# Kernel optimization log

Measured on AMD Instinct MI355X. Metric: run time of the kernel, lower is better.

The kernel has to match this reference:

```python
import jax, jax.numpy as jnp
import numpy as np

N = 50000   # nodes
E = 800000  # edges (avg degree 16)
G = 32      # graphs in batch
IN = 128; HID = 64; H = 2; C = 16
NEG_SLOPE = 0.2
BN_EPS = 1e-5


def setup_inputs() -> dict:
    key = jax.random.key(0)
    ks = jax.random.split(key, 16)
    def rn(k, shape, scale=0.1):
        return jax.random.normal(k, shape, jnp.float32) * scale
    return {
        "feat": jax.random.normal(ks[0], (N, IN), jnp.float32),
        "W0": rn(ks[1], (IN, H * HID)),
        "attn0": rn(ks[2], (H, HID)),
        "W1": rn(ks[3], (H * HID, H * HID)),
        "attn1": rn(ks[4], (H, HID)),
        "W2": rn(ks[5], (H * HID, H * HID)),
        "attn2": rn(ks[6], (H, HID)),
        "Wf": rn(ks[7], (H * HID, H * C)),
        "attnf": rn(ks[8], (H, C)),
        "mlp_w1": rn(ks[9], (C, C)),
        "mlp_gamma": jnp.ones((C,), jnp.float32),
        "mlp_beta": jnp.zeros((C,), jnp.float32),
        "mlp_w2": rn(ks[10], (C, C)),
        "src": jax.random.randint(ks[11], (E,), 0, N, jnp.int32),
        "dst": jax.random.randint(ks[12], (E,), 0, N, jnp.int32),
        "node_graph": jnp.sort(jax.random.randint(ks[13], (N,), 0, G, jnp.int32)),
        "num_graphs": G,
    }


def gatv2_layer(h, src, dst, W, attn, act):
    """DGL GATv2Conv with share_weights=True, bias=False, residual=False."""
    n = h.shape[0]
    nh, d = attn.shape
    z = (h @ W).reshape(n, nh, d)                      # [N,H,D]
    zs = z[src]                                        # [E,H,D] gather (src)
    e = jax.nn.leaky_relu(zs + z[dst], NEG_SLOPE)      # [E,H,D]
    score = jnp.einsum('ehd,hd->eh', e, attn)          # [E,H]
    # edge softmax over incoming edges of dst (shift-invariant max trick)
    m = jax.lax.stop_gradient(jax.ops.segment_max(score, dst, num_segments=n))
    a = jnp.exp(score - m[dst])
    denom = jax.ops.segment_sum(a, dst, num_segments=n)[dst]
    alpha = a / jnp.where(denom == 0, 1.0, denom)      # [E,H]
    out = jax.ops.segment_sum(alpha[..., None] * zs, dst, num_segments=n)  # [N,H,D]
    return act(out) if act is not None else out


def reference(feat, W0, attn0, W1, attn1, W2, attn2, Wf, attnf,
              mlp_w1, mlp_gamma, mlp_beta, mlp_w2,
              src, dst, node_graph, num_graphs):
    relu = jax.nn.relu
    n = feat.shape[0]
    h = gatv2_layer(feat, src, dst, W0, attn0, relu).reshape(n, -1)
    h = gatv2_layer(h, src, dst, W1, attn1, relu).reshape(n, -1)
    h = gatv2_layer(h, src, dst, W2, attn2, relu).reshape(n, -1)
    logits = gatv2_layer(h, src, dst, Wf, attnf, None).mean(axis=1)  # [N,C]
    pooled = jax.ops.segment_sum(logits, node_graph, num_segments=num_graphs)  # [G,C]
    # MLP: relu(batchnorm(lin0(x))) -> lin1 (training-mode batch stats, biased var)
    h1 = pooled @ mlp_w1
    mu = h1.mean(axis=0)
    var = h1.var(axis=0)
    h1 = (h1 - mu) / jnp.sqrt(var + BN_EPS) * mlp_gamma + mlp_beta
    out = relu(h1) @ mlp_w2
    return jax.nn.log_softmax(out, axis=-1)
```

## Files before the change

### kernel.cpp

```cpp
#include <hip/hip_runtime.h>
#include <hip/hip_bf16.h>
#include <hip/hip_fp16.h>
#include <math.h>

#define NN 50000
#define EE 800000
#define GG 32
#define HD 64
#define NHEAD 2
#define CCLS 16
#define NEG_SLOPE 0.2f
#define BN_EPS 1e-5f
#define LOG2E 1.4426950408889634f
#define STRIDE 64

typedef unsigned int u32;
typedef unsigned short u16;
typedef _Float16 hv2 __attribute__((ext_vector_type(2)));
typedef __fp16   cv2 __attribute__((ext_vector_type(2)));

__device__ __forceinline__ hv2 bch2(u32 u) { union { u32 u; hv2 h; } c; c.u = u; return c.h; }
__device__ __forceinline__ u32 bcu32(hv2 h) { union { hv2 h; u32 u; } c; c.h = h; return c.u; }
__device__ __forceinline__ u32 pkrtz(float a, float b) {
    cv2 r = __builtin_amdgcn_cvt_pkrtz(a, b);
    union { cv2 h; u32 u; } c; c.h = r; return c.u;
}
__device__ __forceinline__ hv2 h2max(hv2 a, hv2 b) {
    return __builtin_elementwise_max(a, b);
}
__device__ __forceinline__ float fdot2(hv2 a, hv2 b, float c) {
#if __has_builtin(__builtin_amdgcn_fdot2)
    union { hv2 h; cv2 c2; } ua, ub;
    ua.h = a; ub.h = b;
    return __builtin_amdgcn_fdot2(ua.c2, ub.c2, c, false);
#else
    return fmaf((float)a[0], (float)b[0], fmaf((float)a[1], (float)b[1], c));
#endif
}


__global__ __launch_bounds__(256) void scatter_kernel(const int* __restrict__ src,
                                                      const int* __restrict__ dst,
                                                      int* __restrict__ cursor,
                                                      u16* __restrict__ csr_src) {
    int e = blockIdx.x * 256 + threadIdx.x;
    if (e < EE) {
        int d = dst[e];
        int s = src[e];
        int p = atomicAdd(&cursor[d], 1);
        csr_src[d * STRIDE + p] = (u16)s;
    }
}


template<int KOUT, int RPT, bool F16IN>
__device__ __forceinline__ void gemm_body(const void* __restrict__ hv,
                                          const float* __restrict__ W,
                                          u32* __restrict__ z, int n, int blk) {
    constexpr int CT = KOUT / 8;
    constexpr int RT = 256 / CT;
    constexpr int BR = RT * RPT;
    constexpr int WSTR = (KOUT == 128) ? 140 : (KOUT + 4);
    __shared__ __align__(16) u32 WpD[64 * WSTR];
    __shared__ __align__(16) uint4 hsU4[BR * 17];
    int t = threadIdx.x;
    int row0 = blk * BR;

    for (int i = t; i < 64 * (KOUT / 4); i += 256) {
        int k2 = i / (KOUT / 4), cq = i % (KOUT / 4);
        float4 wa = ((const float4*)W)[(2 * k2) * (KOUT / 4) + cq];
        float4 wb = ((const float4*)W)[(2 * k2 + 1) * (KOUT / 4) + cq];
        uint4 d;
        d.x = pkrtz(wa.x, wb.x); d.y = pkrtz(wa.y, wb.y);
        d.z = pkrtz(wa.z, wb.z); d.w = pkrtz(wa.w, wb.w);
        *(uint4*)&WpD[k2 * WSTR + 4 * cq + ((cq >> 3) << 2)] = d;
    }
    for (int i = t; i < BR * 16; i += 256) {
        int r = i >> 4, c16 = i & 15;
        int gr = row0 + r;
        uint4 u = {0, 0, 0, 0};
        if (gr < n) {
            if (F16IN) {
                u = ((const uint4*)hv)[(size_t)gr * 16 + c16];
            } else {
                float4 f0 = ((const float4*)hv)[(size_t)gr * 32 + 2 * c16];
                float4 f1 = ((const float4*)hv)[(size_t)gr * 32 + 2 * c16 + 1];
                u.x = pkrtz(f0.x, f0.y); u.y = pkrtz(f0.z, f0.w);
                u.z = pkrtz(f1.x, f1.y); u.w = pkrtz(f1.z, f1.w);
            }
        }
        hsU4[r * 17 + c16] = u;
    }
    __syncthreads();

    int tc = t % CT, tr = t / CT;
    float acc[RPT][8];
    #pragma unroll
    for (int i = 0; i < RPT; i++)
        #pragma unroll
        for (int c = 0; c < 8; c++) acc[i][c] = 0.f;

    for (int kq = 0; kq < 16; kq++) {
        uint4 a4[RPT];
        #pragma unroll
        for (int i = 0; i < RPT; i++) a4[i] = hsU4[(tr * RPT + i) * 17 + kq];
        #pragma unroll
        for (int j = 0; j < 4; j++) {
            const u32* wrow = &WpD[(4 * kq + j) * WSTR + tc * 8 + ((tc >> 2) << 2)];
            uint4 wa = *(const uint4*)wrow;
            uint4 wb = *(const uint4*)(wrow + 4);
            u32 wd[8] = {wa.x, wa.y, wa.z, wa.w, wb.x, wb.y, wb.z, wb.w};
            #pragma unroll
            for (int i = 0; i < RPT; i++) {
                u32 av[4] = {a4[i].x, a4[i].y, a4[i].z, a4[i].w};
                hv2 a2 = bch2(av[j]);
                #pragma unroll
                for (int c = 0; c < 8; c++)
                    acc[i][c] = fdot2(a2, bch2(wd[c]), acc[i][c]);
            }
        }
    }
    #pragma unroll
    for (int i = 0; i < RPT; i++) {
        int gr = row0 + tr * RPT + i;
        if (gr < n) {
            uint4 p;
            p.x = pkrtz(acc[i][0], acc[i][1]);
            p.y = pkrtz(acc[i][2], acc[i][3]);
            p.z = pkrtz(acc[i][4], acc[i][5]);
            p.w = pkrtz(acc[i][6], acc[i][7]);
            ((uint4*)z)[(size_t)gr * (KOUT / 8) + tc] = p;
        }
    }
}

template<int KOUT, int RPT, bool F16IN>
__global__ __launch_bounds__(256) void gemm_kernel(const void* __restrict__ hv,
                                                   const float* __restrict__ W,
                                                   u32* __restrict__ z, int n) {
    gemm_body<KOUT, RPT, F16IN>(hv, W, z, n, blockIdx.x);
}

__global__ __launch_bounds__(256) void gemm0_kernel(const void* __restrict__ hv,
                                                    const float* __restrict__ W,
                                                    u32* __restrict__ z,
                                                    int* __restrict__ cursor,
                                                    float* __restrict__ pooled) {
    int gid = blockIdx.x * 256 + threadIdx.x;
    if (gid < NN) cursor[gid] = 0;
    if (gid < GG * CCLS) pooled[gid] = 0.f;
    gemm_body<128, 4, false>(hv, W, z, NN, blockIdx.x);
}


__global__ __launch_bounds__(256) void edge_kernel(const u32* __restrict__ z,
                                                   const float* __restrict__ attn,
                                                   const int* __restrict__ cursor,
                                                   const u16* __restrict__ csr_src,
                                                   u32* __restrict__ out, int n) {
    int wave = blockIdx.x * 4 + (threadIdx.x >> 6);
    int lane = threadIdx.x & 63;
    if (wave >= n) return;
    int i = wave;
    int slot = lane >> 3;
    int q8 = lane & 7;
    const uint4* zr = (const uint4*)z;

    size_t rowi = (size_t)i * 16 + q8 * 2;
    uint4 zua = zr[rowi], zub = zr[rowi + 1];
    hv2 zd[8] = {bch2(zua.x), bch2(zua.y), bch2(zua.z), bch2(zua.w),
                 bch2(zub.x), bch2(zub.y), bch2(zub.z), bch2(zub.w)};
    const float4* af = (const float4*)attn;
    float4 a0 = af[q8 * 4 + 0], a1 = af[q8 * 4 + 1];
    float4 a2 = af[q8 * 4 + 2], a3 = af[q8 * 4 + 3];
    hv2 ah[8] = {bch2(pkrtz(a0.x * LOG2E, a0.y * LOG2E)),
                 bch2(pkrtz(a0.z * LOG2E, a0.w * LOG2E)),
                 bch2(pkrtz(a1.x * LOG2E, a1.y * LOG2E)),
                 bch2(pkrtz(a1.z * LOG2E, a1.w * LOG2E)),
                 bch2(pkrtz(a2.x * LOG2E, a2.y * LOG2E)),
                 bch2(pkrtz(a2.z * LOG2E, a2.w * LOG2E)),
                 bch2(pkrtz(a3.x * LOG2E, a3.y * LOG2E)),
                 bch2(pkrtz(a3.z * LOG2E, a3.w * LOG2E))};
    const hv2 slope2 = {(_Float16)NEG_SLOPE, (_Float16)NEG_SLOPE};

    int deg = cursor[i];
    const u16* ep = csr_src + i * STRIDE;

    float s = 0.f;
    float accf[16];
    #pragma unroll
    for (int j = 0; j < 16; j++) accf[j] = 0.f;

    bool valid = slot < deg;
    int sid = valid ? (int)ep[slot] : i;
    size_t rs = (size_t)sid * 16 + q8 * 2;
    uint4 sa = zr[rs], sb = zr[rs + 1];

    for (int k = 0; k < deg; k += 8) {
        bool more = (k + 8) < deg;
        bool v2 = (k + 8 + slot) < deg;
        uint4 na, nb;
        if (more) {
            int sid2 = v2 ? (int)ep[k + 8 + slot] : i;
            size_t rs2 = (size_t)sid2 * 16 + q8 * 2;
            na = zr[rs2]; nb = zr[rs2 + 1];
        }
        hv2 zs[8] = {bch2(sa.x), bch2(sa.y), bch2(sa.z), bch2(sa.w),
                     bch2(sb.x), bch2(sb.y), bch2(sb.z), bch2(sb.w)};
        float sc = 0.f;
        #pragma unroll
        for (int j = 0; j < 8; j++) {
            hv2 x = zs[j] + zd[j];
            x = h2max(x, x * slope2);
            sc = fdot2(x, ah[j], sc);
        }
        sc += __shfl_xor(sc, 2, 64);
        sc += __shfl_xor(sc, 1, 64);
        float p = valid ? exp2f(sc) : 0.f;
        s += p;
        #pragma unroll
        for (int j = 0; j < 8; j++) {
            accf[2 * j]     = fmaf(p, (float)zs[j][0], accf[2 * j]);
            accf[2 * j + 1] = fmaf(p, (float)zs[j][1], accf[2 * j + 1]);
        }
        sa = na; sb = nb; valid = v2;
    }

    u32 pk[8];
    #pragma unroll
    for (int j = 0; j < 8; j++) pk[j] = pkrtz(accf[2 * j], accf[2 * j + 1]);
    #pragma unroll
    for (int off = 8; off <= 32; off <<= 1) {
        s += __shfl_xor(s, off, 64);
        #pragma unroll
        for (int j = 0; j < 8; j++) {
            u32 o = (u32)__shfl_xor((int)pk[j], off, 64);
            pk[j] = bcu32(bch2(pk[j]) + bch2(o));
        }
    }

    if (slot == 0) {
        float inv = s > 0.f ? 1.f / s : 0.f;
        hv2 inv2 = bch2(pkrtz(inv, inv));
        const hv2 zero2 = {(_Float16)0.f, (_Float16)0.f};
        uint4 pa, pb;
        pa.x = bcu32(h2max(bch2(pk[0]) * inv2, zero2));
        pa.y = bcu32(h2max(bch2(pk[1]) * inv2, zero2));
        pa.z = bcu32(h2max(bch2(pk[2]) * inv2, zero2));
        pa.w = bcu32(h2max(bch2(pk[3]) * inv2, zero2));
        pb.x = bcu32(h2max(bch2(pk[4]) * inv2, zero2));
        pb.y = bcu32(h2max(bch2(pk[5]) * inv2, zero2));
        pb.z = bcu32(h2max(bch2(pk[6]) * inv2, zero2));
        pb.w = bcu32(h2max(bch2(pk[7]) * inv2, zero2));
        ((uint4*)out)[rowi] = pa;
        ((uint4*)out)[rowi + 1] = pb;
    }
}


__global__ __launch_bounds__(256) void edge_final_kernel(const u32* __restrict__ z,
                                                         const float* __restrict__ attn,
                                                         const int* __restrict__ cursor,
                                                         const u16* __restrict__ csr_src,
                                                         const int* __restrict__ node_graph,
                                                         float* __restrict__ pooled, int n) {
    __shared__ float pl[GG * CCLS];
    for (int t = threadIdx.x; t < GG * CCLS; t += 256) pl[t] = 0.f;
    __syncthreads();

    int wave = blockIdx.x * 4 + (threadIdx.x >> 6);
    int lane = threadIdx.x & 63;
    int iv = wave * 2 + (lane >> 5);
    bool mine = iv < n;
    int i = mine ? iv : (n - 1);
    int hl = lane & 31;
    int j = hl >> 3;
    int d8 = hl & 7;
    const uint2* zr = (const uint2*)z;
    uint2 zu = zr[(size_t)i * 8 + d8];
    hv2 zd0 = bch2(zu.x), zd1 = bch2(zu.y);
    float4 av = ((const float4*)attn)[d8];
    hv2 ah0 = bch2(pkrtz(av.x * LOG2E, av.y * LOG2E));
    hv2 ah1 = bch2(pkrtz(av.z * LOG2E, av.w * LOG2E));
    const hv2 slope2 = {(_Float16)NEG_SLOPE, (_Float16)NEG_SLOPE};
    int deg = cursor[i];
    const u16* ep = csr_src + i * STRIDE;

    float s = 0.f;
    float accf[4] = {0.f, 0.f, 0.f, 0.f};
    for (int k = 0; k < deg; k += 4) {
        int kk = k + j;
        bool valid = kk < deg;
        int sid = valid ? (int)ep[kk] : i;
        uint2 su = zr[(size_t)sid * 8 + d8];
        hv2 zs0 = bch2(su.x), zs1 = bch2(su.y);
        hv2 x;
        float sc = 0.f;
        x = zs0 + zd0; x = h2max(x, x * slope2); sc = fdot2(x, ah0, sc);
        x = zs1 + zd1; x = h2max(x, x * slope2); sc = fdot2(x, ah1, sc);
        sc += __shfl_xor(sc, 1, 64);
        sc += __shfl_xor(sc, 2, 64);
        float p = valid ? exp2f(sc) : 0.f;
        s += p;
        accf[0] = fmaf(p, (float)zs0[0], accf[0]);
        accf[1] = fmaf(p, (float)zs0[1], accf[1]);
        accf[2] = fmaf(p, (float)zs1[0], accf[2]);
        accf[3] = fmaf(p, (float)zs1[1], accf[3]);
    }
    #pragma unroll
    for (int off = 8; off <= 16; off <<= 1) {
        s += __shfl_xor(s, off, 64);
        #pragma unroll
        for (int jj = 0; jj < 4; jj++) accf[jj] += __shfl_xor(accf[jj], off, 64);
    }
    float inv = s > 0.f ? 1.f / s : 0.f;
    float4 o;
    o.x = accf[0] * inv; o.y = accf[1] * inv; o.z = accf[2] * inv; o.w = accf[3] * inv;
    o.x = 0.5f * (o.x + __shfl_xor(o.x, 4, 64));
    o.y = 0.5f * (o.y + __shfl_xor(o.y, 4, 64));
    o.z = 0.5f * (o.z + __shfl_xor(o.z, 4, 64));
    o.w = 0.5f * (o.w + __shfl_xor(o.w, 4, 64));
    if (mine && j == 0 && (hl & 4) == 0) {
        int g = node_graph[i];
        float* base = &pl[g * 16 + 4 * d8];
        atomicAdd(&base[0], o.x);
        atomicAdd(&base[1], o.y);
        atomicAdd(&base[2], o.z);
        atomicAdd(&base[3], o.w);
    }
    __syncthreads();
    for (int t = threadIdx.x; t < GG * CCLS; t += 256) {
        float v = pl[t];
        if (v != 0.f) atomicAdd(&pooled[t], v);
    }
}


__global__ __launch_bounds__(512) void mlp_kernel(const float* __restrict__ pooled,
                                                  const float* __restrict__ w1,
                                                  const float* __restrict__ gamma,
                                                  const float* __restrict__ beta,
                                                  const float* __restrict__ w2,
                                                  float* __restrict__ out) {
    __shared__ float P[GG * CCLS], H1[GG * CCLS], H2[GG * CCLS], O[GG * CCLS];
    __shared__ float mu[CCLS], rstd[CCLS], rowm[GG], rowl[GG];
    int t = threadIdx.x;
    int r = t >> 4, c = t & 15;
    if (t < GG * CCLS) P[t] = pooled[t];
    __syncthreads();
    if (t < GG * CCLS) {
        float s = 0.f;
        for (int k = 0; k < 16; k++) s += P[r * 16 + k] * w1[k * 16 + c];
        H1[t] = s;
    }
    __syncthreads();
    if (t < CCLS) {
        float s = 0.f;
        for (int rr = 0; rr < GG; rr++) s += H1[rr * 16 + t];
        float mn = s / GG;
        float s2 = 0.f;
        for (int rr = 0; rr < GG; rr++) { float d = H1[rr * 16 + t] - mn; s2 += d * d; }
        mu[t] = mn; rstd[t] = rsqrtf(s2 / GG + BN_EPS);
    }
    __syncthreads();
    if (t < GG * CCLS) {
        float v = (H1[t] - mu[c]) * rstd[c] * gamma[c] + beta[c];
        H2[t] = fmaxf(v, 0.f);
    }
    __syncthreads();
    if (t < GG * CCLS) {
        float s = 0.f;
        for (int k = 0; k < 16; k++) s += H2[r * 16 + k] * w2[k * 16 + c];
        O[t] = s;
    }
    __syncthreads();
    if (t < GG) {
        float mx = -INFINITY;
        for (int k = 0; k < 16; k++) mx = fmaxf(mx, O[t * 16 + k]);
        float l = 0.f;
        for (int k = 0; k < 16; k++) l += __expf(O[t * 16 + k] - mx);
        rowm[t] = mx; rowl[t] = logf(l);
    }
    __syncthreads();
    if (t < GG * CCLS) out[t] = O[t] - rowm[r] - rowl[r];
}


extern "C" void kernel_launch(void* const* d_in, const int* in_sizes, int n_in,
                              void* d_out, int out_size, void* d_ws, size_t ws_size,
                              hipStream_t stream) {
    const float* feat     = (const float*)d_in[0];
    const float* W0       = (const float*)d_in[1];
    const float* attn0    = (const float*)d_in[2];
    const float* W1       = (const float*)d_in[3];
    const float* attn1    = (const float*)d_in[4];
    const float* W2       = (const float*)d_in[5];
    const float* attn2    = (const float*)d_in[6];
    const float* Wf       = (const float*)d_in[7];
    const float* attnf    = (const float*)d_in[8];
    const float* mlp_w1   = (const float*)d_in[9];
    const float* mlp_g    = (const float*)d_in[10];
    const float* mlp_b    = (const float*)d_in[11];
    const float* mlp_w2   = (const float*)d_in[12];
    const int*   src      = (const int*)d_in[13];
    const int*   dst      = (const int*)d_in[14];
    const int*   ngraph   = (const int*)d_in[15];
    float* out = (float*)d_out;

    char* ws = (char*)d_ws;
    size_t off = 0;
    auto alloc = [&](size_t bytes) {
        void* p = ws + off;
        off = (off + bytes + 255) & ~(size_t)255;
        return p;
    };
    u32* z      = (u32*)alloc((size_t)NN * 64 * sizeof(u32));
    u32* hb0    = (u32*)alloc((size_t)NN * 64 * sizeof(u32));
    u32* hb1    = (u32*)alloc((size_t)NN * 64 * sizeof(u32));
    float* pooled = (float*)alloc(GG * CCLS * sizeof(float));
    int* cursor   = (int*)alloc(NN * sizeof(int));
    u16* csr_src  = (u16*)alloc((size_t)NN * STRIDE * sizeof(u16));

    int edge_grid = (NN + 3) / 4;
    int edgef_grid = (NN + 7) / 8;
    int gemm_grid = (NN + 63) / 64;
    int scat_grid = (EE + 255) / 256;

    gemm0_kernel<<<gemm_grid, 256, 0, stream>>>(feat, W0, z, cursor, pooled);
    scatter_kernel<<<scat_grid, 256, 0, stream>>>(src, dst, cursor, csr_src);
    edge_kernel<<<edge_grid, 256, 0, stream>>>(z, attn0, cursor, csr_src, hb0, NN);

    gemm_kernel<128, 4, true><<<gemm_grid, 256, 0, stream>>>(hb0, W1, z, NN);
    edge_kernel<<<edge_grid, 256, 0, stream>>>(z, attn1, cursor, csr_src, hb1, NN);

    gemm_kernel<128, 4, true><<<gemm_grid, 256, 0, stream>>>(hb1, W2, z, NN);
    edge_kernel<<<edge_grid, 256, 0, stream>>>(z, attn2, cursor, csr_src, hb0, NN);

    gemm_kernel<32, 1, true><<<gemm_grid, 256, 0, stream>>>(hb0, Wf, z, NN);
    edge_final_kernel<<<edgef_grid, 256, 0, stream>>>(z, attnf, cursor, csr_src,
                                                      ngraph, pooled, NN);

    mlp_kernel<<<1, 512, 0, stream>>>(pooled, mlp_w1, mlp_g, mlp_b, mlp_w2, out);
}
```

Measured before the change: 399.9 us.

## Bucket edges by destination before CSR scatter; persistent-grid edge kernel

Result: no change. 407.1 us (+1.8%).

```diff
diff --git a/kernel.cpp b/kernel.cpp
--- a/kernel.cpp
+++ b/kernel.cpp
@@ -13,6 +13,10 @@
 #define BN_EPS 1e-5f
 #define LOG2E 1.4426950408889634f
 #define STRIDE 64
+#define CURB 6250
+#define BUCKCAP 110000
+#define SLICES 392
+#define LCAP 192
 
 typedef unsigned int u32;
 typedef unsigned short u16;
@@ -37,17 +41,65 @@
     return fmaf((float)a[0], (float)b[0], fmaf((float)a[1], (float)b[1], c));
 #endif
 }
-
-
-__global__ __launch_bounds__(256) void scatter_kernel(const int* __restrict__ src,
-                                                      const int* __restrict__ dst,
-                                                      int* __restrict__ cursor,
-                                                      u16* __restrict__ csr_src) {
-    int e = blockIdx.x * 256 + threadIdx.x;
-    if (e < EE) {
-        int d = dst[e];
-        int s = src[e];
-        int p = atomicAdd(&cursor[d], 1);
+__device__ __forceinline__ int curidx(int d) { return (d & 7) * CURB + (d >> 3); }
+
+
+__global__ __launch_bounds__(256) void bucket_kernel(const int* __restrict__ src,
+                                                     const int* __restrict__ dst,
+                                                     int* __restrict__ bcur,
+                                                     u32* __restrict__ buckets,
+                                                     int* __restrict__ cursor,
+                                                     u16* __restrict__ csr_src) {
+    __shared__ int cnt[8], base[8];
+    __shared__ u32 buf[8 * LCAP];
+    int t = threadIdx.x;
+    if (t < 8) cnt[t] = 0;
+    __syncthreads();
+    #pragma unroll
+    for (int q = 0; q < 4; q++) {
+        int e = blockIdx.x * 1024 + q * 256 + t;
+        if (e < EE) {
+            int d = dst[e];
+            int s = src[e];
+            int b = d & 7;
+            int pos = atomicAdd(&cnt[b], 1);
+            if (pos < LCAP) {
+                buf[b * LCAP + pos] = ((u32)d << 16) | (u32)s;
+            } else {
+                int p = atomicAdd(&cursor[curidx(d)], 1);
+                csr_src[d * STRIDE + p] = (u16)s;
+            }
+        }
+    }
+    __syncthreads();
+    if (t < 8) {
+        int c = min(cnt[t], LCAP);
+        cnt[t] = c;
+        base[t] = atomicAdd(&bcur[t], c);
+    }
+    __syncthreads();
+    #pragma unroll
+    for (int b = 0; b < 8; b++) {
+        int c = cnt[b], bs = base[b];
+        for (int i = t; i < c; i += 256)
+            buckets[b * BUCKCAP + bs + i] = buf[b * LCAP + i];
+    }
+}
+
+
+__global__ __launch_bounds__(256) void scatter2_kernel(const u32* __restrict__ buckets,
+                                                       const int* __restrict__ bcur,
+                                                       int* __restrict__ cursor,
+                                                       u16* __restrict__ csr_src) {
+    int b = blockIdx.x & 7;
+    int slice = blockIdx.x >> 3;
+    int cnt = bcur[b];
+    const u32* bp = buckets + b * BUCKCAP;
+    for (int idx = slice * 256 + threadIdx.x; idx < cnt; idx += SLICES * 256) {
+        u32 pk = bp[idx];
+        int d = pk >> 16;
+        int s = pk & 0xffff;
+        int p = atomicAdd(&cursor[b * CURB + (d >> 3)], 1);
         csr_src[d * STRIDE + p] = (u16)s;
     }
 }
@@ -147,29 +199,24 @@
                                                     int* __restrict__ cursor,
                                                     float* __restrict__ pooled) {
     int gid = blockIdx.x * 256 + threadIdx.x;
-    if (gid < NN) cursor[gid] = 0;
+    if (gid < NN + 8) cursor[gid] = 0;
     if (gid < GG * CCLS) pooled[gid] = 0.f;
     gemm_body<128, 4, false>(hv, W, z, NN, blockIdx.x);
 }
 
+
+#define EDGE_BLOCKS 2048
 
 __global__ __launch_bounds__(256) void edge_kernel(const u32* __restrict__ z,
                                                    const float* __restrict__ attn,
                                                    const int* __restrict__ cursor,
                                                    const u16* __restrict__ csr_src,
                                                    u32* __restrict__ out, int n) {
-    int wave = blockIdx.x * 4 + (threadIdx.x >> 6);
     int lane = threadIdx.x & 63;
-    if (wave >= n) return;
-    int i = wave;
     int slot = lane >> 3;
     int q8 = lane & 7;
     const uint4* zr = (const uint4*)z;
 
-    size_t rowi = (size_t)i * 16 + q8 * 2;
-    uint4 zua = zr[rowi], zub = zr[rowi + 1];
-    hv2 zd[8] = {bch2(zua.x), bch2(zua.y), bch2(zua.z), bch2(zua.w),
-                 bch2(zub.x), bch2(zub.y), bch2(zub.z), bch2(zub.w)};
     const float4* af = (const float4*)attn;
     float4 a0 = af[q8 * 4 + 0], a1 = af[q8 * 4 + 1];
     float4 a2 = af[q8 * 4 + 2], a3 = af[q8 * 4 + 3];
@@ -183,77 +230,86 @@
                  bch2(pkrtz(a3.z * LOG2E, a3.w * LOG2E))};
     const hv2 slope2 = {(_Float16)NEG_SLOPE, (_Float16)NEG_SLOPE};
 
-    int deg = cursor[i];
-    const u16* ep = csr_src + i * STRIDE;
-
-    float s = 0.f;
-    float accf[16];
-    #pragma unroll
-    for (int j = 0; j < 16; j++) accf[j] = 0.f;
-
-    bool valid = slot < deg;
-    int sid = valid ? (int)ep[slot] : i;
-    size_t rs = (size_t)sid * 16 + q8 * 2;
-    uint4 sa = zr[rs], sb = zr[rs + 1];
-
-    for (int k = 0; k < deg; k += 8) {
-        bool more = (k + 8) < deg;
-        bool v2 = (k + 8 + slot) < deg;
-        uint4 na, nb;
-        if (more) {
-            int sid2 = v2 ? (int)ep[k + 8 + slot] : i;
-            size_t rs2 = (size_t)sid2 * 16 + q8 * 2;
-            na = zr[rs2]; nb = zr[rs2 + 1];
-        }
-        hv2 zs[8] = {bch2(sa.x), bch2(sa.y), bch2(sa.z), bch2(sa.w),
-                     bch2(sb.x), bch2(sb.y), bch2(sb.z), bch2(sb.w)};
-        float sc = 0.f;
-        #pragma unroll
-        for (int j = 0; j < 8; j++) {
-            hv2 x = zs[j] + zd[j];
-            x = h2max(x, x * slope2);
-            sc = fdot2(x, ah[j], sc);
-        }
-        sc += __shfl_xor(sc, 2, 64);
-        sc += __shfl_xor(sc, 1, 64);
-        float p = valid ? exp2f(sc) : 0.f;
-        s += p;
-        #pragma unroll
-        for (int j = 0; j < 8; j++) {
-            accf[2 * j]     = fmaf(p, (float)zs[j][0], accf[2 * j]);
-            accf[2 * j + 1] = fmaf(p, (float)zs[j][1], accf[2 * j + 1]);
-        }
-        sa = na; sb = nb; valid = v2;
-    }
-
-    u32 pk[8];
-    #pragma unroll
-    for (int j = 0; j < 8; j++) pk[j] = pkrtz(accf[2 * j], accf[2 * j + 1]);
-    #pragma unroll
-    for (int off = 8; off <= 32; off <<= 1) {
-        s += __shfl_xor(s, off, 64);
-        #pragma unroll
-        for (int j = 0; j < 8; j++) {
-            u32 o = (u32)__shfl_xor((int)pk[j], off, 64);
-            pk[j] = bcu32(bch2(pk[j]) + bch2(o));
-        }
-    }
-
-    if (slot == 0) {
-        float inv = s > 0.f ? 1.f / s : 0.f;
-        hv2 inv2 = bch2(pkrtz(inv, inv));
-        const hv2 zero2 = {(_Float16)0.f, (_Float16)0.f};
-        uint4 pa, pb;
-        pa.x = bcu32(h2max(bch2(pk[0]) * inv2, zero2));
-        pa.y = bcu32(h2max(bch2(pk[1]) * inv2, zero2));
-        pa.z = bcu32(h2max(bch2(pk[2]) * inv2, zero2));
-        pa.w = bcu32(h2max(bch2(pk[3]) * inv2, zero2));
-        pb.x = bcu32(h2max(bch2(pk[4]) * inv2, zero2));
-        pb.y = bcu32(h2max(bch2(pk[5]) * inv2, zero2));
-        pb.z = bcu32(h2max(bch2(pk[6]) * inv2, zero2));
-        pb.w = bcu32(h2max(bch2(pk[7]) * inv2, zero2));
-        ((uint4*)out)[rowi] = pa;
-        ((uint4*)out)[rowi + 1] = pb;
+    int wv = blockIdx.x * 4 + (threadIdx.x >> 6);
+    const int NW = EDGE_BLOCKS * 4;
+
+    for (int i = wv; i < n; i += NW) {
+        size_t rowi = (size_t)i * 16 + q8 * 2;
+        uint4 zua = zr[rowi], zub = zr[rowi + 1];
+        hv2 zd[8] = {bch2(zua.x), bch2(zua.y), bch2(zua.z), bch2(zua.w),
+                     bch2(zub.x), bch2(zub.y), bch2(zub.z), bch2(zub.w)};
+        int deg = cursor[curidx(i)];
+        const u16* ep = csr_src + i * STRIDE;
+
+        float s = 0.f;
+        float accf[16];
+        #pragma unroll
+        for (int j = 0; j < 16; j++) accf[j] = 0.f;
+
+        bool valid = slot < deg;
+        int sid = valid ? (int)ep[slot] : i;
+        size_t rs = (size_t)sid * 16 + q8 * 2;
+        uint4 sa = zr[rs], sb = zr[rs + 1];
+
+        for (int k = 0; k < deg; k += 8) {
+            bool more = (k + 8) < deg;
+            bool v2 = (k + 8 + slot) < deg;
+            uint4 na, nb;
+            if (more) {
+                int sid2 = v2 ? (int)ep[k + 8 + slot] : i;
+                size_t rs2 = (size_t)sid2 * 16 + q8 * 2;
+                na = zr[rs2]; nb = zr[rs2 + 1];
+            }
+            hv2 zs[8] = {bch2(sa.x), bch2(sa.y), bch2(sa.z), bch2(sa.w),
+                         bch2(sb.x), bch2(sb.y), bch2(sb.z), bch2(sb.w)};
+            float sc = 0.f;
+            #pragma unroll
+            for (int j = 0; j < 8; j++) {
+                hv2 x = zs[j] + zd[j];
+                x = h2max(x, x * slope2);
+                sc = fdot2(x, ah[j], sc);
+            }
+            sc += __shfl_xor(sc, 2, 64);
+            sc += __shfl_xor(sc, 1, 64);
+            float p = valid ? exp2f(sc) : 0.f;
+            s += p;
+            #pragma unroll
+            for (int j = 0; j < 8; j++) {
+                accf[2 * j]     = fmaf(p, (float)zs[j][0], accf[2 * j]);
+                accf[2 * j + 1] = fmaf(p, (float)zs[j][1], accf[2 * j + 1]);
+            }
+            sa = na; sb = nb; valid = v2;
+        }
+
+        u32 pk[8];
+        #pragma unroll
+        for (int j = 0; j < 8; j++) pk[j] = pkrtz(accf[2 * j], accf[2 * j + 1]);
+        #pragma unroll
+        for (int off = 8; off <= 32; off <<= 1) {
+            s += __shfl_xor(s, off, 64);
+            #pragma unroll
+            for (int j = 0; j < 8; j++) {
+                u32 o = (u32)__shfl_xor((int)pk[j], off, 64);
+                pk[j] = bcu32(bch2(pk[j]) + bch2(o));
+            }
+        }
+
+        if (slot == 0) {
+            float inv = s > 0.f ? 1.f / s : 0.f;
+            hv2 inv2 = bch2(pkrtz(inv, inv));
+            const hv2 zero2 = {(_Float16)0.f, (_Float16)0.f};
+            uint4 pa, pb;
+            pa.x = bcu32(h2max(bch2(pk[0]) * inv2, zero2));
+            pa.y = bcu32(h2max(bch2(pk[1]) * inv2, zero2));
+            pa.z = bcu32(h2max(bch2(pk[2]) * inv2, zero2));
+            pa.w = bcu32(h2max(bch2(pk[3]) * inv2, zero2));
+            pb.x = bcu32(h2max(bch2(pk[4]) * inv2, zero2));
+            pb.y = bcu32(h2max(bch2(pk[5]) * inv2, zero2));
+            pb.z = bcu32(h2max(bch2(pk[6]) * inv2, zero2));
+            pb.w = bcu32(h2max(bch2(pk[7]) * inv2, zero2));
+            ((uint4*)out)[rowi] = pa;
+            ((uint4*)out)[rowi + 1] = pb;
+        }
     }
 }
 
@@ -283,7 +339,7 @@
     hv2 ah0 = bch2(pkrtz(av.x * LOG2E, av.y * LOG2E));
     hv2 ah1 = bch2(pkrtz(av.z * LOG2E, av.w * LOG2E));
     const hv2 slope2 = {(_Float16)NEG_SLOPE, (_Float16)NEG_SLOPE};
-    int deg = cursor[i];
+    int deg = cursor[curidx(i)];
     const u16* ep = csr_src + i * STRIDE;
 
     float s = 0.f;
@@ -418,23 +474,25 @@
     u32* hb0    = (u32*)alloc((size_t)NN * 64 * sizeof(u32));
     u32* hb1    = (u32*)alloc((size_t)NN * 64 * sizeof(u32));
     float* pooled = (float*)alloc(GG * CCLS * sizeof(float));
-    int* cursor   = (int*)alloc(NN * sizeof(int));
+    int* cursor   = (int*)alloc((NN + 8) * sizeof(int));
+    int* bcur     = cursor + NN;
     u16* csr_src  = (u16*)alloc((size_t)NN * STRIDE * sizeof(u16));
-
-    int edge_grid = (NN + 3) / 4;
+    u32* buckets  = (u32*)alloc((size_t)8 * BUCKCAP * sizeof(u32));
+
     int edgef_grid = (NN + 7) / 8;
     int gemm_grid = (NN + 63) / 64;
-    int scat_grid = (EE + 255) / 256;
+    int buck_grid = (EE + 1023) / 1024;
 
     gemm0_kernel<<<gemm_grid, 256, 0, stream>>>(feat, W0, z, cursor, pooled);
-    scatter_kernel<<<scat_grid, 256, 0, stream>>>(src, dst, cursor, csr_src);
-    edge_kernel<<<edge_grid, 256, 0, stream>>>(z, attn0, cursor, csr_src, hb0, NN);
+    bucket_kernel<<<buck_grid, 256, 0, stream>>>(src, dst, bcur, buckets, cursor, csr_src);
+    scatter2_kernel<<<8 * SLICES, 256, 0, stream>>>(buckets, bcur, cursor, csr_src);
+    edge_kernel<<<EDGE_BLOCKS, 256, 0, stream>>>(z, attn0, cursor, csr_src, hb0, NN);
 
     gemm_kernel<128, 4, true><<<gemm_grid, 256, 0, stream>>>(hb0, W1, z, NN);
-    edge_kernel<<<edge_grid, 256, 0, stream>>>(z, attn1, cursor, csr_src, hb1, NN);
+    edge_kernel<<<EDGE_BLOCKS, 256, 0, stream>>>(z, attn1, cursor, csr_src, hb1, NN);
 
     gemm_kernel<128, 4, true><<<gemm_grid, 256, 0, stream>>>(hb1, W2, z, NN);
-    edge_kernel<<<edge_grid, 256, 0, stream>>>(z, attn2, cursor, csr_src, hb0, NN);
+    edge_kernel<<<EDGE_BLOCKS, 256, 0, stream>>>(z, attn2, cursor, csr_src, hb0, NN);
 
     gemm_kernel<32, 1, true><<<gemm_grid, 256, 0, stream>>>(hb0, Wf, z, NN);
     edge_final_kernel<<<edgef_grid, 256, 0, stream>>>(z, attnf, cursor, csr_src,
```
